# Performance work log

Measured on AMD Instinct MI355X. Metric: run time of the kernel, lower is better.

The kernel has to match this reference:

```python
import jax, jax.numpy as jnp
import numpy as np

B, S, D, H = 4, 1024, 1024, 16
HD = D // H  # head_dim = 64


def setup_inputs() -> dict:
    key = jax.random.key(0)
    ks = jax.random.split(key, 12)
    std = 1.0 / np.sqrt(D)
    inp = {
        "query": jax.random.normal(ks[0], (B, S, D), jnp.float32),
        "key": jax.random.normal(ks[1], (B, S, D), jnp.float32),
        "value": jax.random.normal(ks[2], (B, S, D), jnp.float32),
        # four Linear(embed_dim, embed_dim) layers: q, k, v, out
        "Wq": jax.random.normal(ks[3], (D, D), jnp.float32) * std,
        "bq": jnp.zeros((D,), jnp.float32),
        "Wk": jax.random.normal(ks[4], (D, D), jnp.float32) * std,
        "bk": jnp.zeros((D,), jnp.float32),
        "Wv": jax.random.normal(ks[5], (D, D), jnp.float32) * std,
        "bv": jnp.zeros((D,), jnp.float32),
        "Wo": jax.random.normal(ks[6], (D, D), jnp.float32) * std,
        "bo": jnp.zeros((D,), jnp.float32),
        # compressor: Linear(num_heads, 1)
        "Wc": jax.random.normal(ks[7], (H,), jnp.float32) / np.sqrt(H),
        "bc": jnp.zeros((), jnp.float32),
    }
    return inp


def reference(query, key, value, Wq, bq, Wk, bk, Wv, bv, Wo, bo, Wc, bc):
    b, s, d = query.shape
    h, hd = H, HD

    def proj(x, W, bias):
        # [b,s,d] @ [d,d] -> [b,h,s,hd]
        y = jnp.einsum('bsd,de->bse', x, W) + bias
        return y.reshape(b, s, h, hd).transpose(0, 2, 1, 3)

    q = proj(query, Wq, bq)
    k = proj(key, Wk, bk)
    v = proj(value, Wv, bv)

    scores = jnp.einsum('bhqd,bhkd->bhqk', q, k) / np.sqrt(hd)
    p_attn = jax.nn.softmax(scores, axis=-1)  # [b,h,s,s]; dropout is identity in eval

    x = jnp.einsum('bhqk,bhkd->bhqd', p_attn, v)
    x = x.transpose(0, 2, 1, 3).reshape(b, s, d)
    out = jnp.einsum('bsd,de->bse', x, Wo) + bo

    # head compression: Linear(num_heads, 1) over head axis -> [b,1,s,s]
    attn_c = (jnp.einsum('bhqk,h->bqk', p_attn, Wc) + bc)[:, None, :, :]
    return out, attn_c
```

## Files before the change

kernel.cpp:

```cpp
#include <hip/hip_runtime.h>
#include <hip/hip_bf16.h>

#define SS 1024
#define DD 1024
#define HH 16
#define HDh 64

typedef short bf16x8 __attribute__((ext_vector_type(8)));
typedef float f32x4 __attribute__((ext_vector_type(4)));

__device__ inline unsigned short f2bf(float f) {
    union { __hip_bfloat16 h; unsigned short u; } cv;
    cv.h = __float2bfloat16(f);
    return cv.u;
}
__device__ inline float bf2f(short u) {
    unsigned int x = ((unsigned int)(unsigned short)u) << 16;
    return __uint_as_float(x);
}

#define PIN4(a, b, c, d) asm volatile("" : "+v"(a), "+v"(b), "+v"(c), "+v"(d))

__device__ inline void gload_lds16(const unsigned short* g, unsigned short* l) {
    __builtin_amdgcn_global_load_lds(
        (const __attribute__((address_space(1))) unsigned int*)g,
        (__attribute__((address_space(3))) unsigned int*)l, 16, 0, 0);
}

__global__ __launch_bounds__(256) void cvt3(
    const float* __restrict__ a, const float* __restrict__ b, const float* __restrict__ c,
    unsigned short* __restrict__ oa, unsigned short* __restrict__ ob, unsigned short* __restrict__ oc)
{
    size_t i = ((size_t)blockIdx.x * 256 + threadIdx.x) * 4;
    float4 va = *(const float4*)(a + i);
    float4 vb = *(const float4*)(b + i);
    float4 vc = *(const float4*)(c + i);
    *(ushort4*)(oa + i) = make_ushort4(f2bf(va.x), f2bf(va.y), f2bf(va.z), f2bf(va.w));
    *(ushort4*)(ob + i) = make_ushort4(f2bf(vb.x), f2bf(vb.y), f2bf(vb.z), f2bf(vb.w));
    *(ushort4*)(oc + i) = make_ushort4(f2bf(vc.x), f2bf(vc.y), f2bf(vc.z), f2bf(vc.w));
}

__global__ __launch_bounds__(256) void wtrans(
    const float* __restrict__ Wq, const float* __restrict__ Wk,
    const float* __restrict__ Wv, const float* __restrict__ Wo,
    unsigned short* __restrict__ oq, unsigned short* __restrict__ ok,
    unsigned short* __restrict__ ov, unsigned short* __restrict__ oo)
{
    __shared__ float tile[32][33];
    int z = blockIdx.z;
    const float* W = z == 0 ? Wq : (z == 1 ? Wk : (z == 2 ? Wv : Wo));
    unsigned short* O = z == 0 ? oq : (z == 1 ? ok : (z == 2 ? ov : oo));
    int e0 = blockIdx.x * 32, d0 = blockIdx.y * 32;
    int r = threadIdx.x >> 3, c4 = (threadIdx.x & 7) * 4;
    float4 v = *(const float4*)(W + (size_t)(d0 + r) * DD + e0 + c4);
    tile[r][c4 + 0] = v.x; tile[r][c4 + 1] = v.y; tile[r][c4 + 2] = v.z; tile[r][c4 + 3] = v.w;
    __syncthreads();
    ushort4 u = make_ushort4(f2bf(tile[c4 + 0][r]), f2bf(tile[c4 + 1][r]),
                             f2bf(tile[c4 + 2][r]), f2bf(tile[c4 + 3][r]));
    *(ushort4*)(O + (size_t)(e0 + r) * DD + d0 + c4) = u;
}

__device__ inline void gemm128_core(const unsigned short* __restrict__ A,
                                    const unsigned short* __restrict__ Bt,
                                    const float* __restrict__ bias,
                                    void* __restrict__ out, int mode, float oscale,
                                    int m0, int n0)
{
    __shared__ unsigned short As[128 * 32];
    __shared__ unsigned short Bs[128 * 32];
    int t = threadIdx.x;
    int w = t >> 6, lane = t & 63, quad = lane >> 4, l15 = lane & 15;
    int wm = w >> 1, wn = w & 1;

    f32x4 zero = {0.f, 0.f, 0.f, 0.f};
    f32x4 acc[4][4];
#pragma unroll
    for (int i = 0; i < 4; i++)
#pragma unroll
        for (int j = 0; j < 4; j++) acc[i][j] = zero;

    for (int k0 = 0; k0 < DD; k0 += 32) {
        __syncthreads();
#pragma unroll
        for (int i = 0; i < 4; i++) {
            int chunk = w + i * 4;
            int half = chunk >> 3;
            int c = chunk & 7;
            const unsigned short* g = (half ? Bt : A)
                + (size_t)((half ? n0 : m0) + c * 16 + (lane >> 2)) * DD + k0 + (lane & 3) * 8;
            unsigned short* l = (half ? Bs : As) + c * 512 + lane * 8;
            gload_lds16(g, l);
        }
        __syncthreads();
        bf16x8 af[4], bfr[4];
#pragma unroll
        for (int mi = 0; mi < 4; mi++)
            af[mi] = *(const bf16x8*)&As[(wm * 64 + mi * 16 + l15) * 32 + quad * 8];
#pragma unroll
        for (int ni = 0; ni < 4; ni++)
            bfr[ni] = *(const bf16x8*)&Bs[(wn * 64 + ni * 16 + l15) * 32 + quad * 8];
#pragma unroll
        for (int mi = 0; mi < 4; mi++)
#pragma unroll
            for (int ni = 0; ni < 4; ni++)
                acc[mi][ni] = __builtin_amdgcn_mfma_f32_16x16x32_bf16(af[mi], bfr[ni], acc[mi][ni], 0, 0, 0);
    }

#pragma unroll
    for (int mi = 0; mi < 4; mi++)
#pragma unroll
        for (int ni = 0; ni < 4; ni++) {
            int n = n0 + wn * 64 + ni * 16 + l15;
            float bv = bias[n];
#pragma unroll
            for (int r = 0; r < 4; r++) {
                int m = m0 + wm * 64 + mi * 16 + quad * 4 + r;
                float v = (acc[mi][ni][r] + bv) * oscale;
                if (mode == 2) {
                    ((float*)out)[(size_t)m * DD + n] = v;
                } else {
                    int bb = m >> 10, s = m & 1023, hh = n >> 6, d = n & 63;
                    size_t head = (size_t)(bb * HH + hh) << 16;
                    size_t off;
                    if (mode == 0) {
                        off = head + (((size_t)(s >> 4) * 2 + (d >> 5)) * 64
                              + ((d >> 3) & 3) * 16 + (s & 15)) * 8 + (d & 7);
                    } else {
                        off = head + (((size_t)(s >> 5) * 4 + (d >> 4)) * 64
                              + ((s >> 3) & 3) * 16 + (d & 15)) * 8 + (s & 7);
                    }
                    ((unsigned short*)out)[off] = f2bf(v);
                }
            }
        }
}

#define SCLQ 0.18033688f

__global__ __launch_bounds__(256, 3) void gemm_qkv(
    const unsigned short* __restrict__ xq, const unsigned short* __restrict__ xk,
    const unsigned short* __restrict__ xv,
    const unsigned short* __restrict__ wtq, const unsigned short* __restrict__ wtk,
    const unsigned short* __restrict__ wtv,
    const float* __restrict__ bq, const float* __restrict__ bk, const float* __restrict__ bv,
    unsigned short* __restrict__ q, unsigned short* __restrict__ k, unsigned short* __restrict__ v)
{
    int bid = blockIdx.x;
    int swz = (bid & 7) * 96 + (bid >> 3);
    int z = swz >> 8, rem = swz & 255;
    int n0 = (rem & 7) * 128, m0 = (rem >> 3) * 128;
    const unsigned short* A  = z == 0 ? xq  : (z == 1 ? xk  : xv);
    const unsigned short* Bt = z == 0 ? wtq : (z == 1 ? wtk : wtv);
    const float* bias        = z == 0 ? bq  : (z == 1 ? bk  : bv);
    void* out                = z == 0 ? (void*)q : (z == 1 ? (void*)k : (void*)v);
    gemm128_core(A, Bt, bias, out, z == 2 ? 1 : 0, z == 0 ? SCLQ : 1.0f, m0, n0);
}

__global__ __launch_bounds__(256, 3) void gemm_o(
    const unsigned short* __restrict__ x, const unsigned short* __restrict__ wto,
    const float* __restrict__ bo, float* __restrict__ out)
{
    int bid = blockIdx.x;
    int swz = (bid & 7) * 32 + (bid >> 3);
    int n0 = (swz & 7) * 128, m0 = (swz >> 3) * 128;
    gemm128_core(x, wto, bo, out, 2, 1.0f, m0, n0);
}


__global__ __launch_bounds__(256, 2) void fattn_kernel(
    const unsigned short* __restrict__ qf, const unsigned short* __restrict__ kf,
    const unsigned short* __restrict__ vf, float* __restrict__ Z,
    unsigned short* __restrict__ xat)
{
    __shared__ __align__(16) unsigned short plds[4][1280];
    int t = threadIdx.x, w = t >> 6, lane = t & 63, quad = lane >> 4, l15 = lane & 15;
    int bid = blockIdx.x;
    int swz = (bid & 7) * 64 + (bid >> 3);
    int bh = swz >> 3, m0 = (swz & 7) * 128;
    int b = bh >> 4, h = bh & 15;
    const unsigned short* qh = qf + ((size_t)bh << 16);
    const unsigned short* kh = kf + ((size_t)bh << 16);
    const unsigned short* vh = vf + ((size_t)bh << 16);

    bf16x8 qfrag[2][2];
    int s16b = (m0 >> 4) + w * 2;
#pragma unroll
    for (int mi = 0; mi < 2; mi++)
#pragma unroll
        for (int dh = 0; dh < 2; dh++)
            qfrag[mi][dh] = *(const bf16x8*)(qh + (size_t)((s16b + mi) * 2 + dh) * 512 + lane * 8);

    f32x4 zero = {0.f, 0.f, 0.f, 0.f};
    f32x4 oacc[2][4];
#pragma unroll
    for (int mi = 0; mi < 2; mi++)
#pragma unroll
        for (int ni = 0; ni < 4; ni++) oacc[mi][ni] = zero;
    float zacc[2] = {0.f, 0.f};

    bf16x8 kc[4], vc[4];
#pragma unroll
    for (int i = 0; i < 4; i++) {
        kc[i] = *(const bf16x8*)(kh + (size_t)i * 512 + lane * 8);
        vc[i] = *(const bf16x8*)(vh + (size_t)i * 512 + lane * 8);
    }

    for (int kt = 0; kt < 32; kt++) {
        int nk = kt < 31 ? kt + 1 : 31;
        bf16x8 kn[4], vn[4];
#pragma unroll
        for (int i = 0; i < 4; i++) {
            kn[i] = *(const bf16x8*)(kh + ((size_t)nk * 4 + i) * 512 + lane * 8);
            vn[i] = *(const bf16x8*)(vh + ((size_t)nk * 4 + i) * 512 + lane * 8);
        }
        PIN4(kn[0], kn[1], kn[2], kn[3]);
        PIN4(vn[0], vn[1], vn[2], vn[3]);

        f32x4 st[2][2];
#pragma unroll
        for (int si = 0; si < 2; si++)
#pragma unroll
            for (int mi = 0; mi < 2; mi++) {
                st[si][mi] = __builtin_amdgcn_mfma_f32_16x16x32_bf16(kc[si * 2 + 0], qfrag[mi][0], zero, 0, 0, 0);
                st[si][mi] = __builtin_amdgcn_mfma_f32_16x16x32_bf16(kc[si * 2 + 1], qfrag[mi][1], st[si][mi], 0, 0, 0);
            }

#pragma unroll
        for (int mi = 0; mi < 2; mi++)
#pragma unroll
            for (int si = 0; si < 2; si++) {
                float p0 = exp2f(st[si][mi][0]);
                float p1 = exp2f(st[si][mi][1]);
                float p2 = exp2f(st[si][mi][2]);
                float p3 = exp2f(st[si][mi][3]);
                zacc[mi] += (p0 + p1) + (p2 + p3);
                unsigned int pk0 = (unsigned int)f2bf(p0) | ((unsigned int)f2bf(p1) << 16);
                unsigned int pk1 = (unsigned int)f2bf(p2) | ((unsigned int)f2bf(p3) << 16);
                *(uint2*)&plds[w][(mi * 16 + l15) * 40 + si * 16 + quad * 4] = make_uint2(pk0, pk1);
            }
        bf16x8 pa[2];
#pragma unroll
        for (int mi = 0; mi < 2; mi++)
            pa[mi] = *(const bf16x8*)&plds[w][(mi * 16 + l15) * 40 + quad * 8];

#pragma unroll
        for (int mi = 0; mi < 2; mi++)
#pragma unroll
            for (int ni = 0; ni < 4; ni++)
                oacc[mi][ni] = __builtin_amdgcn_mfma_f32_16x16x32_bf16(pa[mi], vc[ni], oacc[mi][ni], 0, 0, 0);

#pragma unroll
        for (int i = 0; i < 4; i++) { kc[i] = kn[i]; vc[i] = vn[i]; }
    }

    float zt[2];
#pragma unroll
    for (int mi = 0; mi < 2; mi++) {
        float s = zacc[mi];
        s += __shfl_xor(s, 16);
        s += __shfl_xor(s, 32);
        zt[mi] = s;
        if (quad == 0)
            Z[(size_t)bh * 1024 + m0 + w * 32 + mi * 16 + l15] = s;
    }

#pragma unroll
    for (int mi = 0; mi < 2; mi++)
#pragma unroll
        for (int r = 0; r < 4; r++) {
            int qrow = quad * 4 + r;
            float iz = 1.f / __shfl(zt[mi], qrow);
            int q = m0 + w * 32 + mi * 16 + qrow;
#pragma unroll
            for (int ni = 0; ni < 4; ni++)
                xat[((size_t)(b * 1024 + q)) * 1024 + h * 64 + ni * 16 + l15] =
                    f2bf(oacc[mi][ni][r] * iz);
        }
}

__global__ __launch_bounds__(512, 2) void attc_kernel(
    const unsigned short* __restrict__ qf, const unsigned short* __restrict__ kf,
    const float* __restrict__ Z, const float* __restrict__ Wc,
    const float* __restrict__ bcp, float* __restrict__ attc)
{
    int t = threadIdx.x, w = t >> 6, lane = t & 63, quad = lane >> 4, l15 = lane & 15;
    int bid = blockIdx.x;
    int swz = (bid & 7) * 32 + (bid >> 3);
    int b = swz >> 6, qb = (swz >> 3) & 7, kb = swz & 7;
    int qt = qb * 8 + w;
    int q = qt * 16 + l15;
    float bc = *bcp;
    f32x4 zero = {0.f, 0.f, 0.f, 0.f};
    f32x4 acc[4][2];
#pragma unroll
    for (int kt = 0; kt < 4; kt++)
#pragma unroll
        for (int si = 0; si < 2; si++) acc[kt][si] = zero;

    for (int h = 0; h < 16; h++) {
        int bh = b * 16 + h;
        const unsigned short* qh = qf + ((size_t)bh << 16);
        const unsigned short* kh = kf + ((size_t)bh << 16);
        bf16x8 qfr0 = *(const bf16x8*)(qh + (size_t)(qt * 2 + 0) * 512 + lane * 8);
        bf16x8 qfr1 = *(const bf16x8*)(qh + (size_t)(qt * 2 + 1) * 512 + lane * 8);
        float wz = Wc[h] / Z[(size_t)bh * 1024 + q];
#pragma unroll
        for (int kt = 0; kt < 4; kt++) {
            int akt = kb * 4 + kt;
            bf16x8 kfr[4];
#pragma unroll
            for (int i = 0; i < 4; i++)
                kfr[i] = *(const bf16x8*)(kh + ((size_t)akt * 4 + i) * 512 + lane * 8);
#pragma unroll
            for (int si = 0; si < 2; si++) {
                f32x4 st = __builtin_amdgcn_mfma_f32_16x16x32_bf16(kfr[si * 2 + 0], qfr0, zero, 0, 0, 0);
                st = __builtin_amdgcn_mfma_f32_16x16x32_bf16(kfr[si * 2 + 1], qfr1, st, 0, 0, 0);
#pragma unroll
                for (int r = 0; r < 4; r++)
                    acc[kt][si][r] += wz * exp2f(st[r]);
            }
        }
    }
#pragma unroll
    for (int kt = 0; kt < 4; kt++)
#pragma unroll
        for (int si = 0; si < 2; si++) {
            float4 vv = make_float4(acc[kt][si][0] + bc, acc[kt][si][1] + bc,
                                    acc[kt][si][2] + bc, acc[kt][si][3] + bc);
            *(float4*)(attc + ((size_t)(b * 1024 + q)) * 1024 + kb * 128 + kt * 32 + si * 16 + quad * 4) = vv;
        }
}

#define LDK(f) (*(const bf16x8*)(kh + ((size_t)(f) * 64 + lane) * 8))
#define LDV(f) (*(const bf16x8*)(vh + ((size_t)(f) * 64 + lane) * 8))

__global__ __launch_bounds__(1024, 4) void attn_kernel(
    const unsigned short* __restrict__ qf, const unsigned short* __restrict__ kf,
    const unsigned short* __restrict__ vf, const float* __restrict__ Wc,
    const float* __restrict__ bcp, unsigned short* __restrict__ xout,
    float* __restrict__ attc)
{
    __shared__ float accc[16][1028];
    __shared__ unsigned short tsc[16][16][36];

    int t = threadIdx.x, w = t >> 6, lane = t & 63, quad = lane >> 4, l15 = lane & 15;
    int b = blockIdx.x >> 6, qt = blockIdx.x & 63;
    int h = w;

    for (int i = t; i < 16 * 1028; i += 1024) (&accc[0][0])[i] = 0.f;
    __syncthreads();

    const unsigned short* qh = qf + ((size_t)(b * HH + h) << 16);
    const unsigned short* kh = kf + ((size_t)(b * HH + h) << 16);
    const unsigned short* vh = vf + ((size_t)(b * HH + h) << 16);
    float wc = Wc[h], bc = *bcp;
    f32x4 zero = {0.f, 0.f, 0.f, 0.f};

    bf16x8 a0 = *(const bf16x8*)(qh + ((size_t)(qt * 2 + 0) * 64 + lane) * 8);
    bf16x8 a1 = *(const bf16x8*)(qh + ((size_t)(qt * 2 + 1) * 64 + lane) * 8);

    float rs[4] = {0.f, 0.f, 0.f, 0.f};
    bf16x8 c0 = LDK(0), c1 = LDK(1), c2 = LDK(2), c3 = LDK(3);
    PIN4(c0, c1, c2, c3);
    bf16x8 d0 = LDK(4), d1 = LDK(5), d2 = LDK(6), d3 = LDK(7);
    PIN4(d0, d1, d2, d3);
#pragma unroll 2
    for (int g = 0; g < 32; g++) {
        int gn = g < 30 ? g + 2 : 31;
        bf16x8 n0 = LDK(gn * 4 + 0), n1 = LDK(gn * 4 + 1);
        bf16x8 n2 = LDK(gn * 4 + 2), n3 = LDK(gn * 4 + 3);
        PIN4(n0, n1, n2, n3);
        f32x4 s0 = zero, s1 = zero;
        s0 = __builtin_amdgcn_mfma_f32_16x16x32_bf16(a0, c0, s0, 0, 0, 0);
        s0 = __builtin_amdgcn_mfma_f32_16x16x32_bf16(a1, c1, s0, 0, 0, 0);
        s1 = __builtin_amdgcn_mfma_f32_16x16x32_bf16(a0, c2, s1, 0, 0, 0);
        s1 = __builtin_amdgcn_mfma_f32_16x16x32_bf16(a1, c3, s1, 0, 0, 0);
#pragma unroll
        for (int r = 0; r < 4; r++) rs[r] += exp2f(s0[r]) + exp2f(s1[r]);
        c0 = d0; c1 = d1; c2 = d2; c3 = d3;
        d0 = n0; d1 = n1; d2 = n2; d3 = n3;
    }
#pragma unroll
    for (int r = 0; r < 4; r++) {
        rs[r] += __shfl_xor(rs[r], 1);
        rs[r] += __shfl_xor(rs[r], 2);
        rs[r] += __shfl_xor(rs[r], 4);
        rs[r] += __shfl_xor(rs[r], 8);
    }
    float invC[4], sC[4];
#pragma unroll
    for (int r = 0; r < 4; r++) { invC[r] = 1.f / rs[r]; sC[r] = wc * invC[r]; }

    f32x4 o0 = zero, o1 = zero, o2 = zero, o3 = zero;
    int cc0 = (2 * w) & 31;
    bf16x8 k0 = LDK(cc0 * 4 + 0), k1 = LDK(cc0 * 4 + 1);
    bf16x8 k2 = LDK(cc0 * 4 + 2), k3 = LDK(cc0 * 4 + 3);
    PIN4(k0, k1, k2, k3);
    bf16x8 v0 = LDV(cc0 * 4 + 0), v1 = LDV(cc0 * 4 + 1);
    bf16x8 v2 = LDV(cc0 * 4 + 2), v3 = LDV(cc0 * 4 + 3);
    PIN4(v0, v1, v2, v3);
#pragma unroll 2
    for (int i = 0; i < 32; i++) {
        int cc = (i + 2 * w) & 31;
        int cn = ((i + 1) + 2 * w) & 31;
        bf16x8 kn0 = LDK(cn * 4 + 0), kn1 = LDK(cn * 4 + 1);
        bf16x8 kn2 = LDK(cn * 4 + 2), kn3 = LDK(cn * 4 + 3);
        PIN4(kn0, kn1, kn2, kn3);
        bf16x8 vn0 = LDV(cn * 4 + 0), vn1 = LDV(cn * 4 + 1);
        bf16x8 vn2 = LDV(cn * 4 + 2), vn3 = LDV(cn * 4 + 3);
        PIN4(vn0, vn1, vn2, vn3);

        f32x4 s0 = zero, s1 = zero;
        s0 = __builtin_amdgcn_mfma_f32_16x16x32_bf16(a0, k0, s0, 0, 0, 0);
        s0 = __builtin_amdgcn_mfma_f32_16x16x32_bf16(a1, k1, s0, 0, 0, 0);
        s1 = __builtin_amdgcn_mfma_f32_16x16x32_bf16(a0, k2, s1, 0, 0, 0);
        s1 = __builtin_amdgcn_mfma_f32_16x16x32_bf16(a1, k3, s1, 0, 0, 0);

#pragma unroll
        for (int r = 0; r < 4; r++) {
            float p0 = exp2f(s0[r]);
            float p1 = exp2f(s1[r]);
            int row = quad * 4 + r;
            tsc[w][row][l15] = f2bf(p0);
            tsc[w][row][16 + l15] = f2bf(p1);
            atomicAdd(&accc[row][cc * 32 + l15], sC[r] * p0);
            atomicAdd(&accc[row][cc * 32 + 16 + l15], sC[r] * p1);
        }
        bf16x8 ap = *(const bf16x8*)&tsc[w][l15][quad * 8];

        o0 = __builtin_amdgcn_mfma_f32_16x16x32_bf16(ap, v0, o0, 0, 0, 0);
        o1 = __builtin_amdgcn_mfma_f32_16x16x32_bf16(ap, v1, o1, 0, 0, 0);
        o2 = __builtin_amdgcn_mfma_f32_16x16x32_bf16(ap, v2, o2, 0, 0, 0);
        o3 = __builtin_amdgcn_mfma_f32_16x16x32_bf16(ap, v3, o3, 0, 0, 0);
        k0 = kn0; k1 = kn1; k2 = kn2; k3 = kn3;
        v0 = vn0; v1 = vn1; v2 = vn2; v3 = vn3;
    }

    f32x4 oo[4] = {o0, o1, o2, o3};
#pragma unroll
    for (int j = 0; j < 4; j++)
#pragma unroll
        for (int r = 0; r < 4; r++) {
            int row = quad * 4 + r;
            xout[((size_t)(b * SS) + qt * 16 + row) * DD + h * 64 + j * 16 + l15] =
                f2bf(oo[j][r] * invC[r]);
        }

    __syncthreads();
    for (int i = t; i < 16 * 1024; i += 1024) {
        int row = i >> 10, col = i & 1023;
        attc[((size_t)b * SS + qt * 16 + row) * SS + col] = accc[row][col] + bc;
    }
}

extern "C" void kernel_launch(void* const* d_in, const int* in_sizes, int n_in,
                              void* d_out, int out_size, void* d_ws, size_t ws_size,
                              hipStream_t stream) {
    const float* query = (const float*)d_in[0];
    const float* key   = (const float*)d_in[1];
    const float* value = (const float*)d_in[2];
    const float* Wq = (const float*)d_in[3];
    const float* bq = (const float*)d_in[4];
    const float* Wk = (const float*)d_in[5];
    const float* bk = (const float*)d_in[6];
    const float* Wv = (const float*)d_in[7];
    const float* bv = (const float*)d_in[8];
    const float* Wo = (const float*)d_in[9];
    const float* bo = (const float*)d_in[10];
    const float* Wc = (const float*)d_in[11];
    const float* bc = (const float*)d_in[12];

    unsigned short* ws  = (unsigned short*)d_ws;
    unsigned short* xq  = ws;
    unsigned short* xk  = xq  + (size_t)4194304;
    unsigned short* xv  = xk  + (size_t)4194304;
    unsigned short* wtq = xv  + (size_t)4194304;
    unsigned short* wtk = wtq + (size_t)1048576;
    unsigned short* wtv = wtk + (size_t)1048576;
    unsigned short* wto = wtv + (size_t)1048576;
    unsigned short* qfb = wto + (size_t)1048576;
    unsigned short* kfb = qfb + (size_t)4194304;
    unsigned short* vfb = kfb + (size_t)4194304;
    unsigned short* xat = vfb + (size_t)4194304;

    float* out0 = (float*)d_out;
    float* attc = out0 + (size_t)4194304;

    const size_t base_bytes = 67108864;
    const size_t z_bytes = 262144;
    bool fast = ws_size >= base_bytes + z_bytes;

    hipLaunchKernelGGL(cvt3, dim3(4096), dim3(256), 0, stream,
                       query, key, value, xq, xk, xv);
    hipLaunchKernelGGL(wtrans, dim3(32, 32, 4), dim3(256), 0, stream,
                       Wq, Wk, Wv, Wo, wtq, wtk, wtv, wto);
    hipLaunchKernelGGL(gemm_qkv, dim3(768), dim3(256), 0, stream,
                       xq, xk, xv, wtq, wtk, wtv, bq, bk, bv, qfb, kfb, vfb);

    if (fast) {
        float* Zbuf = (float*)((char*)d_ws + base_bytes);
        hipLaunchKernelGGL(fattn_kernel, dim3(512), dim3(256), 0, stream,
                           qfb, kfb, vfb, Zbuf, xat);
        hipLaunchKernelGGL(attc_kernel, dim3(256), dim3(512), 0, stream,
                           qfb, kfb, Zbuf, Wc, bc, attc);
    } else {
        hipLaunchKernelGGL(attn_kernel, dim3(256), dim3(1024), 0, stream,
                           qfb, kfb, vfb, Wc, bc, xat, attc);
    }

    hipLaunchKernelGGL(gemm_o, dim3(256), dim3(256), 0, stream,
                       xat, wto, bo, out0);
}
```

Baseline: 253.7 us.

## Double-buffer GEMM LDS staging, merge prep kernels, fuse output GEMM into tail

Merges the activation conversion and weight transpose into one launch. Gives the shared 128x128 GEMM core double-buffered LDS staging with XOR-swizzled columns, prefetching the next k-slice before computing the current one. Runs the output projection GEMM as extra blocks of the attention-compression kernel, so the two independent tail workloads share one launch and can overlap. Risks: extra LDS use, idle threads in the 512-thread GEMM blocks, and tight hand-written waitcnt/barrier ordering.

```diff
diff --git a/kernel.cpp b/kernel.cpp
--- a/kernel.cpp
+++ b/kernel.cpp
@@ -27,37 +27,57 @@
         (__attribute__((address_space(3))) unsigned int*)l, 16, 0, 0);
 }
 
-__global__ __launch_bounds__(256) void cvt3(
+__global__ __launch_bounds__(256) void prep(
     const float* __restrict__ a, const float* __restrict__ b, const float* __restrict__ c,
-    unsigned short* __restrict__ oa, unsigned short* __restrict__ ob, unsigned short* __restrict__ oc)
-{
-    size_t i = ((size_t)blockIdx.x * 256 + threadIdx.x) * 4;
-    float4 va = *(const float4*)(a + i);
-    float4 vb = *(const float4*)(b + i);
-    float4 vc = *(const float4*)(c + i);
-    *(ushort4*)(oa + i) = make_ushort4(f2bf(va.x), f2bf(va.y), f2bf(va.z), f2bf(va.w));
-    *(ushort4*)(ob + i) = make_ushort4(f2bf(vb.x), f2bf(vb.y), f2bf(vb.z), f2bf(vb.w));
-    *(ushort4*)(oc + i) = make_ushort4(f2bf(vc.x), f2bf(vc.y), f2bf(vc.z), f2bf(vc.w));
-}
-
-__global__ __launch_bounds__(256) void wtrans(
+    unsigned short* __restrict__ oa, unsigned short* __restrict__ ob, unsigned short* __restrict__ oc,
     const float* __restrict__ Wq, const float* __restrict__ Wk,
     const float* __restrict__ Wv, const float* __restrict__ Wo,
-    unsigned short* __restrict__ oq, unsigned short* __restrict__ ok,
+    unsigned short* __restrict__ oq, unsigned short* __restrict__ okk,
     unsigned short* __restrict__ ov, unsigned short* __restrict__ oo)
 {
     __shared__ float tile[32][33];
-    int z = blockIdx.z;
-    const float* W = z == 0 ? Wq : (z == 1 ? Wk : (z == 2 ? Wv : Wo));
-    unsigned short* O = z == 0 ? oq : (z == 1 ? ok : (z == 2 ? ov : oo));
-    int e0 = blockIdx.x * 32, d0 = blockIdx.y * 32;
-    int r = threadIdx.x >> 3, c4 = (threadIdx.x & 7) * 4;
-    float4 v = *(const float4*)(W + (size_t)(d0 + r) * DD + e0 + c4);
-    tile[r][c4 + 0] = v.x; tile[r][c4 + 1] = v.y; tile[r][c4 + 2] = v.z; tile[r][c4 + 3] = v.w;
-    __syncthreads();
-    ushort4 u = make_ushort4(f2bf(tile[c4 + 0][r]), f2bf(tile[c4 + 1][r]),
-                             f2bf(tile[c4 + 2][r]), f2bf(tile[c4 + 3][r]));
-    *(ushort4*)(O + (size_t)(e0 + r) * DD + d0 + c4) = u;
+    int bid = blockIdx.x;
+    if (bid < 4096) {
+        size_t i = ((size_t)bid * 256 + threadIdx.x) * 4;
+        float4 va = *(const float4*)(a + i);
+        float4 vb = *(const float4*)(b + i);
+        float4 vc = *(const float4*)(c + i);
+        *(ushort4*)(oa + i) = make_ushort4(f2bf(va.x), f2bf(va.y), f2bf(va.z), f2bf(va.w));
+        *(ushort4*)(ob + i) = make_ushort4(f2bf(vb.x), f2bf(vb.y), f2bf(vb.z), f2bf(vb.w));
+        *(ushort4*)(oc + i) = make_ushort4(f2bf(vc.x), f2bf(vc.y), f2bf(vc.z), f2bf(vc.w));
+    } else {
+        int idx = bid - 4096;
+        int z = idx >> 10;
+        const float* W = z == 0 ? Wq : (z == 1 ? Wk : (z == 2 ? Wv : Wo));
+        unsigned short* O = z == 0 ? oq : (z == 1 ? okk : (z == 2 ? ov : oo));
+        int e0 = (idx & 31) * 32, d0 = ((idx >> 5) & 31) * 32;
+        int r = threadIdx.x >> 3, c4 = (threadIdx.x & 7) * 4;
+        float4 v = *(const float4*)(W + (size_t)(d0 + r) * DD + e0 + c4);
+        tile[r][c4 + 0] = v.x; tile[r][c4 + 1] = v.y; tile[r][c4 + 2] = v.z; tile[r][c4 + 3] = v.w;
+        __syncthreads();
+        ushort4 u = make_ushort4(f2bf(tile[c4 + 0][r]), f2bf(tile[c4 + 1][r]),
+                                 f2bf(tile[c4 + 2][r]), f2bf(tile[c4 + 3][r]));
+        *(ushort4*)(O + (size_t)(e0 + r) * DD + d0 + c4) = u;
+    }
+}
+
+__device__ inline void stage128(const unsigned short* __restrict__ A,
+                                const unsigned short* __restrict__ Bt,
+                                int m0, int n0, int k0,
+                                unsigned short* As, unsigned short* Bs,
+                                int w, int lane)
+{
+    int colg = (lane & 3) ^ ((lane >> 2) & 3) ^ ((lane >> 4) & 3);
+#pragma unroll
+    for (int i = 0; i < 4; i++) {
+        int chunk = w + i * 4;
+        int half = chunk >> 3;
+        int c = chunk & 7;
+        const unsigned short* g = (half ? Bt : A)
+            + (size_t)((half ? n0 : m0) + c * 16 + (lane >> 2)) * DD + k0 + colg * 8;
+        unsigned short* l = (half ? Bs : As) + c * 512 + lane * 8;
+        gload_lds16(g, l);
+    }
 }
 
 __device__ inline void gemm128_core(const unsigned short* __restrict__ A,
@@ -66,11 +86,13 @@
                                     void* __restrict__ out, int mode, float oscale,
                                     int m0, int n0)
 {
-    __shared__ unsigned short As[128 * 32];
-    __shared__ unsigned short Bs[128 * 32];
+    __shared__ unsigned short As[2][4096];
+    __shared__ unsigned short Bs[2][4096];
     int t = threadIdx.x;
+    bool act = t < 256;
     int w = t >> 6, lane = t & 63, quad = lane >> 4, l15 = lane & 15;
     int wm = w >> 1, wn = w & 1;
+    int fsw = (l15 & 3) ^ ((l15 >> 2) & 3);
 
     f32x4 zero = {0.f, 0.f, 0.f, 0.f};
     f32x4 acc[4][4];
@@ -79,33 +101,40 @@
 #pragma unroll
         for (int j = 0; j < 4; j++) acc[i][j] = zero;
 
+    if (act) stage128(A, Bt, m0, n0, 0, As[0], Bs[0], w, lane);
+
+    int cur = 0;
     for (int k0 = 0; k0 < DD; k0 += 32) {
-        __syncthreads();
-#pragma unroll
-        for (int i = 0; i < 4; i++) {
-            int chunk = w + i * 4;
-            int half = chunk >> 3;
-            int c = chunk & 7;
-            const unsigned short* g = (half ? Bt : A)
-                + (size_t)((half ? n0 : m0) + c * 16 + (lane >> 2)) * DD + k0 + (lane & 3) * 8;
-            unsigned short* l = (half ? Bs : As) + c * 512 + lane * 8;
-            gload_lds16(g, l);
-        }
-        __syncthreads();
-        bf16x8 af[4], bfr[4];
-#pragma unroll
-        for (int mi = 0; mi < 4; mi++)
-            af[mi] = *(const bf16x8*)&As[(wm * 64 + mi * 16 + l15) * 32 + quad * 8];
-#pragma unroll
-        for (int ni = 0; ni < 4; ni++)
-            bfr[ni] = *(const bf16x8*)&Bs[(wn * 64 + ni * 16 + l15) * 32 + quad * 8];
-#pragma unroll
-        for (int mi = 0; mi < 4; mi++)
+        if (act) {
+            if (k0 + 32 < DD) {
+                stage128(A, Bt, m0, n0, k0 + 32, As[cur ^ 1], Bs[cur ^ 1], w, lane);
+                asm volatile("s_waitcnt vmcnt(4)" ::: "memory");
+            } else {
+                asm volatile("s_waitcnt vmcnt(0)" ::: "memory");
+            }
+        }
+        __builtin_amdgcn_s_barrier();
+        __builtin_amdgcn_sched_barrier(0);
+        if (act) {
+            bf16x8 af[4], bfr[4];
+#pragma unroll
+            for (int mi = 0; mi < 4; mi++)
+                af[mi] = *(const bf16x8*)&As[cur][(wm * 64 + mi * 16 + l15) * 32 + (quad ^ fsw) * 8];
 #pragma unroll
             for (int ni = 0; ni < 4; ni++)
-                acc[mi][ni] = __builtin_amdgcn_mfma_f32_16x16x32_bf16(af[mi], bfr[ni], acc[mi][ni], 0, 0, 0);
-    }
-
+                bfr[ni] = *(const bf16x8*)&Bs[cur][(wn * 64 + ni * 16 + l15) * 32 + (quad ^ fsw) * 8];
+#pragma unroll
+            for (int mi = 0; mi < 4; mi++)
+#pragma unroll
+                for (int ni = 0; ni < 4; ni++)
+                    acc[mi][ni] = __builtin_amdgcn_mfma_f32_16x16x32_bf16(af[mi], bfr[ni], acc[mi][ni], 0, 0, 0);
+        }
+        __builtin_amdgcn_sched_barrier(0);
+        __builtin_amdgcn_s_barrier();
+        cur ^= 1;
+    }
+
+    if (!act) return;
 #pragma unroll
     for (int mi = 0; mi < 4; mi++)
 #pragma unroll
@@ -278,11 +307,20 @@
         }
 }
 
-__global__ __launch_bounds__(512, 2) void attc_kernel(
+__global__ __launch_bounds__(512, 2) void tail_kernel(
     const unsigned short* __restrict__ qf, const unsigned short* __restrict__ kf,
     const float* __restrict__ Z, const float* __restrict__ Wc,
-    const float* __restrict__ bcp, float* __restrict__ attc)
-{
+    const float* __restrict__ bcp, float* __restrict__ attc,
+    const unsigned short* __restrict__ xat, const unsigned short* __restrict__ wto,
+    const float* __restrict__ bo, float* __restrict__ out0)
+{
+    if (blockIdx.x >= 256) {
+        int bid2 = blockIdx.x - 256;
+        int swz = (bid2 & 7) * 32 + (bid2 >> 3);
+        int n0 = (swz & 7) * 128, m0 = (swz >> 3) * 128;
+        gemm128_core(xat, wto, bo, out0, 2, 1.0f, m0, n0);
+        return;
+    }
     int t = threadIdx.x, w = t >> 6, lane = t & 63, quad = lane >> 4, l15 = lane & 15;
     int bid = blockIdx.x;
     int swz = (bid & 7) * 32 + (bid >> 3);
@@ -490,9 +528,8 @@
     const size_t z_bytes = 262144;
     bool fast = ws_size >= base_bytes + z_bytes;
 
-    hipLaunchKernelGGL(cvt3, dim3(4096), dim3(256), 0, stream,
-                       query, key, value, xq, xk, xv);
-    hipLaunchKernelGGL(wtrans, dim3(32, 32, 4), dim3(256), 0, stream,
+    hipLaunchKernelGGL(prep, dim3(8192), dim3(256), 0, stream,
+                       query, key, value, xq, xk, xv,
                        Wq, Wk, Wv, Wo, wtq, wtk, wtv, wto);
     hipLaunchKernelGGL(gemm_qkv, dim3(768), dim3(256), 0, stream,
                        xq, xk, xv, wtq, wtk, wtv, bq, bk, bv, qfb, kfb, vfb);
@@ -501,13 +538,13 @@
         float* Zbuf = (float*)((char*)d_ws + base_bytes);
         hipLaunchKernelGGL(fattn_kernel, dim3(512), dim3(256), 0, stream,
                            qfb, kfb, vfb, Zbuf, xat);
-        hipLaunchKernelGGL(attc_kernel, dim3(256), dim3(512), 0, stream,
-                           qfb, kfb, Zbuf, Wc, bc, attc);
+        hipLaunchKernelGGL(tail_kernel, dim3(512), dim3(512), 0, stream,
+                           qfb, kfb, Zbuf, Wc, bc, attc,
+                           xat, wto, bo, out0);
     } else {
         hipLaunchKernelGGL(attn_kernel, dim3(256), dim3(1024), 0, stream,
                            qfb, kfb, vfb, Wc, bc, xat, attc);
-    }
-
-    hipLaunchKernelGGL(gemm_o, dim3(256), dim3(256), 0, stream,
-                       xat, wto, bo, out0);
-}
+        hipLaunchKernelGGL(gemm_o, dim3(256), dim3(256), 0, stream,
+                           xat, wto, bo, out0);
+    }
+}
```

Result: faster. 236.7 us (-6.7%).
